# Performance work log

Hardware: AMD Instinct MI355X
Metric: run time of the kernel (lower is better)

The kernel has to match this reference:

```python
import jax, jax.numpy as jnp
import numpy as np

_SAMPLING_EPS = 1e-5


def setup_inputs() -> dict:
    key = jax.random.key(0)
    ks = jax.random.split(key, 7)
    N, V, H = 256, 128000, 200  # num_seqs, vocab_size, output-history length
    logits = jax.random.normal(ks[0], (N, V), dtype=jnp.float32)
    output_tokens = jax.random.randint(ks[1], (N, H), 0, V, dtype=jnp.int32)
    presence_penalties = jax.random.uniform(ks[2], (N,), jnp.float32, 0.0, 2.0)
    frequency_penalties = jax.random.uniform(ks[3], (N,), jnp.float32, 0.0, 2.0)
    temperatures = jax.random.uniform(ks[4], (N,), jnp.float32, 0.5, 1.5)
    top_ps = jax.random.uniform(ks[5], (N,), jnp.float32, 0.5, 1.0)
    top_ks = jax.random.randint(ks[6], (N,), 1, 1000, dtype=jnp.int32)
    return {
        "logits": logits,
        "presence_penalties": presence_penalties,
        "frequency_penalties": frequency_penalties,
        "temperatures": temperatures,
        "top_ps": top_ps,
        "output_tokens": output_tokens,
        "top_ks": top_ks,
    }


def reference(logits, presence_penalties, frequency_penalties, temperatures,
              top_ps, output_tokens, top_ks):
    N, V = logits.shape

    # ---- _apply_penalties: bincount of previously generated tokens per row ----
    rows = jnp.arange(N)[:, None]  # [N,1] broadcast against [N,H] token ids
    bin_counts = jnp.zeros((N, V), logits.dtype).at[rows, output_tokens].add(1.0)
    # rows are skipped when both penalties are < eps (original builds an index list)
    active = ((presence_penalties >= _SAMPLING_EPS) |
              (frequency_penalties >= _SAMPLING_EPS))[:, None]
    presence_mask = (bin_counts > 0.0).astype(logits.dtype)
    penalty = (frequency_penalties[:, None] * bin_counts
               + presence_penalties[:, None] * presence_mask)
    logits = logits - jnp.where(active, penalty, jnp.zeros((), logits.dtype))

    # ---- temperature scaling + softmax ----
    logits = logits / temperatures[:, None]
    probs = jax.nn.softmax(logits, axis=-1)

    # ---- _apply_top_p_top_k: sort desc, cumsum, mask, unsort ----
    probs_idx = jnp.argsort(-probs, axis=-1)                    # descending order
    probs_sort = jnp.take_along_axis(probs, probs_idx, axis=-1)
    probs_sum = jnp.cumsum(probs_sort, axis=-1)
    top_p_mask = (probs_sum - probs_sort) > top_ps[:, None]     # exclusive cumsum > p
    probs_sort = jnp.where(top_p_mask, 0.0, probs_sort)
    top_k_mask = jnp.arange(V, dtype=top_ks.dtype)[None, :] >= top_ks[:, None]
    probs_sort = jnp.where(top_k_mask, 0.0, probs_sort)
    inv_idx = jnp.argsort(probs_idx, axis=-1)                   # unsort permutation
    filtered_probs = jnp.take_along_axis(probs_sort, inv_idx, axis=-1)
    return filtered_probs
```

## Files before the change

kernel.cpp:

```cpp
#include <hip/hip_runtime.h>
#include <stdint.h>

#define NB 8192
#define BSHIFT 19
#define HS 512
#define HM 511
#define CAP 4096
#define CAP2 6144
#define PCAP 2048
#define NRB 2048
#define NT 1024
#define CAPTHR 1.75f

typedef unsigned long long ull;

__device__ __forceinline__ void bar_lds() {
    asm volatile("s_waitcnt lgkmcnt(0)" ::: "memory");
    __builtin_amdgcn_s_barrier();
    __builtin_amdgcn_sched_barrier(0);
}

__device__ __forceinline__ unsigned mono_u32(float x) {
    unsigned b = __float_as_uint(x);
    return (b & 0x80000000u) ? ~b : (b | 0x80000000u);
}
__device__ __forceinline__ float inv_mono(unsigned u) {
    unsigned b = (u & 0x80000000u) ? (u & 0x7fffffffu) : ~u;
    return __uint_as_float(b);
}

__device__ __forceinline__ float compute_x(float l, int cnt,
                                           float pres, float freq, float t) {
    float pen = __fadd_rn(__fmul_rn(freq, (float)cnt), (cnt > 0) ? pres : 0.0f);
    return __fdiv_rn(__fsub_rn(l, pen), t);
}

#define SHFL_STAGE(kk, jj) do {                                              \
    int _s = (jj) >> 1;                                                      \
    ull _pA = __shfl_xor(A, _s), _pB = __shfl_xor(B, _s);                    \
    bool _keepmn = (((e0 & (jj)) == 0) == ((e0 & (kk)) != 0));               \
    ull _mnA = (A < _pA) ? A : _pA, _mxA = (A < _pA) ? _pA : A;              \
    ull _mnB = (B < _pB) ? B : _pB, _mxB = (B < _pB) ? _pB : B;              \
    A = _keepmn ? _mnA : _mxA;  B = _keepmn ? _mnB : _mxB;                   \
} while (0)
#define PAIR_STAGE(kk) do {                                                  \
    bool _up = ((e0 & (kk)) != 0);                                           \
    ull _mn = (A < B) ? A : B, _mx = (A < B) ? B : A;                        \
    A = _up ? _mn : _mx;  B = _up ? _mx : _mn;                               \
} while (0)
#define ZDRIB(nn) do {                                                       \
    for (int _z = 0; _z < (nn) && zc < ZITER; ++_z) {                        \
        int _p = tid + zc * NT; if (_p < V4) o4p[_p] = z4; ++zc;             \
    }                                                                        \
} while (0)

__global__ __launch_bounds__(NT) void k_fused(
    const float* __restrict__ logits, const int* __restrict__ tokens,
    const float* __restrict__ pres_v, const float* __restrict__ freq_v,
    const float* __restrict__ temps, const float* __restrict__ topp_v,
    const int* __restrict__ topk_v, int V, int H, float* __restrict__ out)
{
    __shared__ __align__(16) char smem[(32 + 16 + 8 + 4) * 1024];
    unsigned* hc = (unsigned*)smem;
    ull* skey = (ull*)smem;
    char* regB = smem + 32 * 1024;
    float* se = (float*)regB;
    ull* tmpc = (ull*)regB;
    char* regC = smem + 48 * 1024;
    unsigned* rh = (unsigned*)regC;
    unsigned* cbuf = (unsigned*)regB;
    char* regD = smem + 56 * 1024;
    int* hkey = (int*)regD;
    int* hval = (int*)(regD + 2 * 1024);
    __shared__ int wt_i[16];
    __shared__ float wt_f[16];
    __shared__ float esum_s, corr_s;
    __shared__ int bstar_s, lcnt_s, rb_s, pcnt_s, cap_s;

    int row = blockIdx.x, tid = threadIdx.x;
    int lane = tid & 63, wid = tid >> 6;
    for (int b = tid; b < NB; b += NT) hc[b] = 0u;
    if (tid == 0) {
        esum_s = 0.f; corr_s = 0.f; bstar_s = -1;
        lcnt_s = 0; rb_s = 0; pcnt_s = 0; cap_s = 0;
    }

    for (int i = tid; i < HS; i += NT) { hkey[i] = -1; hval[i] = 0; }
    __syncthreads();
    const int* trow = tokens + (size_t)row * H;
    for (int i = tid; i < H; i += NT) {
        int v = trow[i];
        unsigned h = ((unsigned)v * 2654435761u) >> 23;
        while (true) {
            int prev = atomicCAS(&hkey[h], -1, v);
            if (prev == -1 || prev == v) { atomicAdd(&hval[h], 1); break; }
            h = (h + 1) & HM;
        }
    }
    __syncthreads();

    float t = temps[row];
    float topp = topp_v[row];
    float r = __fdiv_rn(1.0f, t);
    const float* lrow = logits + (size_t)row * V;
    const float4* l4p = (const float4*)lrow;
    float4* o4p = (float4*)(out + (size_t)row * V);
    const float4 z4 = make_float4(0.f, 0.f, 0.f, 0.f);
    int V4 = V >> 2;
    int ZITER = (V4 + NT - 1) / NT;
    int zc = 0;

    float es = 0.0f;
    int i = tid;
    for (; i + 7 * NT < V4; i += 8 * NT) {
        float4 arr[8];
#pragma unroll
        for (int q = 0; q < 8; ++q) arr[q] = l4p[i + q * NT];
#pragma unroll
        for (int q = 0; q < 8; ++q) {
            int vb = (i + q * NT) << 2;
#pragma unroll
            for (int j = 0; j < 4; ++j) {
                float l = (&arr[q].x)[j];
                float x = __fmul_rn(l, r);
                atomicAdd(&hc[mono_u32(x) >> BSHIFT], 1u);
                es += __expf(x);
                if (l >= CAPTHR) {
                    int pos = atomicAdd(&cap_s, 1);
                    if (pos < CAP2) cbuf[pos] = (unsigned)(vb + j);
                }
            }
        }
    }
    for (; i < V4; i += NT) {
        float4 A4 = l4p[i];
#pragma unroll
        for (int j = 0; j < 4; ++j) {
            float l = (&A4.x)[j];
            float x = __fmul_rn(l, r);
            atomicAdd(&hc[mono_u32(x) >> BSHIFT], 1u);
            es += __expf(x);
            if (l >= CAPTHR) {
                int pos = atomicAdd(&cap_s, 1);
                if (pos < CAP2) cbuf[pos] = (unsigned)((i << 2) + j);
            }
        }
    }
    for (int v = (V4 << 2) + tid; v < V; v += NT) {
        float l = lrow[v];
        float x = __fmul_rn(l, r);
        atomicAdd(&hc[mono_u32(x) >> BSHIFT], 1u);
        es += __expf(x);
        if (l >= CAPTHR) {
            int pos = atomicAdd(&cap_s, 1);
            if (pos < CAP2) cbuf[pos] = (unsigned)v;
        }
    }
    for (int off = 32; off; off >>= 1) es += __shfl_down(es, off);
    if ((tid & 63) == 0) atomicAdd(&esum_s, es);
    __syncthreads();

    float pres = pres_v[row], freq = freq_v[row];
    int active = (pres >= 1e-5f) || (freq >= 1e-5f);
    float corr = 0.0f;
    if (active) {
        for (int s = tid; s < HS; s += NT) {
            int v = hkey[s];
            if (v >= 0) {
                int c = hval[s];
                float l = lrow[v];
                float x0 = __fmul_rn(l, r);
                float xp = compute_x(l, c, pres, freq, t);
                unsigned b0 = mono_u32(x0) >> BSHIFT;
                unsigned bp = mono_u32(xp) >> BSHIFT;
                if (b0 != bp) { atomicSub(&hc[b0], 1u); atomicAdd(&hc[bp], 1u); }
                corr += __expf(xp) - __expf(x0);
            }
        }
    }
    for (int off = 32; off; off >>= 1) corr += __shfl_down(corr, off);
    if ((tid & 63) == 0) atomicAdd(&corr_s, corr);
    __syncthreads();

    const int BPT = NB / NT;
    int base = tid * BPT;
    int acc = 0;
#pragma unroll
    for (int q = BPT - 1; q >= 0; --q) { acc += (int)hc[base + q]; hc[base + q] = (unsigned)acc; }
    int k = topk_v[row];
    {
        int v = acc;
#pragma unroll
        for (int off = 1; off < 64; off <<= 1) {
            int o = __shfl_down(v, off);
            if (lane + off < 64) v += o;
        }
        if (lane == 0) wt_i[wid] = v;
        __syncthreads();
        int above = v - acc;
#pragma unroll
        for (int w = 0; w < 16; ++w) if (w > wid) above += wt_i[w];
        int best = -1;
#pragma unroll
        for (int q = BPT - 1; q >= 0; --q)
            if ((int)hc[base + q] + above >= k) { best = base + q; break; }
        if (best >= 0) atomicMax(&bstar_s, best);
    }
    __syncthreads();
    int bst = bstar_s - 2;
    if (bst < 0) bst = 0;
    float Sp = esum_s + corr_s;
    int ccount = cap_s;
    __syncthreads();

    int lb = (int)(mono_u32(__fmul_rn(CAPTHR, r)) >> BSHIFT);
    bool skip_c = (ccount <= CAP2) && (lb < bst);

    if (skip_c) {
        unsigned myidx[6];
#pragma unroll
        for (int q = 0; q < 6; ++q) {
            int j2 = tid + q * NT;
            myidx[q] = (j2 < ccount) ? cbuf[j2] : 0xffffffffu;
        }
        float myl[6];
#pragma unroll
        for (int q = 0; q < 6; ++q)
            if (myidx[q] != 0xffffffffu) myl[q] = lrow[myidx[q]];
#pragma unroll
        for (int q = 0; q < 6; ++q) {
            if (myidx[q] != 0xffffffffu) {
                float l = myl[q];
                unsigned ua = mono_u32(__fmul_rn(l, r));
                if ((int)(ua >> BSHIFT) >= bst) {
                    unsigned ue = mono_u32(__fdiv_rn(l, t));
                    int pos = atomicAdd(&lcnt_s, 1);
                    if (pos < CAP)
                        skey[pos] = ((ull)ue << 32) | (unsigned)~myidx[q];
                }
            }
        }
    } else {
        i = tid;
        for (; i + 7 * NT < V4; i += 8 * NT) {
            float4 arr[8];
#pragma unroll
            for (int q = 0; q < 8; ++q) arr[q] = l4p[i + q * NT];
#pragma unroll
            for (int q = 0; q < 8; ++q) {
                int vb = (i + q * NT) << 2;
#pragma unroll
                for (int j = 0; j < 4; ++j) {
                    float l = (&arr[q].x)[j];
                    unsigned ua = mono_u32(__fmul_rn(l, r));
                    if ((int)(ua >> BSHIFT) >= bst) {
                        unsigned ue = mono_u32(__fdiv_rn(l, t));
                        int pos = atomicAdd(&lcnt_s, 1);
                        if (pos < CAP)
                            skey[pos] = ((ull)ue << 32) | (unsigned)~(unsigned)(vb + j);
                    }
                }
            }
        }
        for (; i < V4; i += NT) {
            float4 A4 = l4p[i];
#pragma unroll
            for (int j = 0; j < 4; ++j) {
                float l = (&A4.x)[j];
                unsigned ua = mono_u32(__fmul_rn(l, r));
                if ((int)(ua >> BSHIFT) >= bst) {
                    unsigned ue = mono_u32(__fdiv_rn(l, t));
                    int pos = atomicAdd(&lcnt_s, 1);
                    if (pos < CAP)
                        skey[pos] = ((ull)ue << 32) | (unsigned)~(unsigned)((i << 2) + j);
                }
            }
        }
        for (int v = (V4 << 2) + tid; v < V; v += NT) {
            float l = lrow[v];
            unsigned ua = mono_u32(__fmul_rn(l, r));
            if ((int)(ua >> BSHIFT) >= bst) {
                unsigned ue = mono_u32(__fdiv_rn(l, t));
                int pos = atomicAdd(&lcnt_s, 1);
                if (pos < CAP)
                    skey[pos] = ((ull)ue << 32) | (unsigned)~(unsigned)v;
            }
        }
    }
    __syncthreads();
    int count = lcnt_s; if (count > CAP) count = CAP;

    if (active) {
        for (int j = tid; j < count; j += NT) {
            unsigned idx = ~(unsigned)(skey[j] & 0xffffffffull);
            unsigned h = (idx * 2654435761u) >> 23;
            int c = 0;
            while (true) {
                int kk = hkey[h];
                if (kk == (int)idx) { c = hval[h]; break; }
                if (kk == -1) break;
                h = (h + 1) & HM;
            }
            if (c > 0) {
                float xp = compute_x(lrow[idx], c, pres, freq, t);
                skey[j] = ((ull)mono_u32(xp) << 32) | (unsigned)~idx;
            }
        }
    }
    ZDRIB(2); bar_lds();

    for (int g = tid; g < NRB; g += NT) rh[g] = 0u;
    ZDRIB(2); bar_lds();
    int gmin = bst << 6;
    for (int j = tid; j < count; j += NT) {
        unsigned u = (unsigned)(skey[j] >> 32);
        int rel = (int)(u >> 13) - gmin;
        rel = rel < 0 ? 0 : (rel > NRB - 1 ? NRB - 1 : rel);
        atomicAdd(&rh[rel], 1u);
    }
    ZDRIB(2); bar_lds();
    {
        int b2i = tid * 2;
        int a2 = (int)rh[b2i + 1];
        rh[b2i + 1] = (unsigned)a2;
        a2 += (int)rh[b2i];
        rh[b2i] = (unsigned)a2;
        int v = a2;
#pragma unroll
        for (int off = 1; off < 64; off <<= 1) {
            int o = __shfl_down(v, off);
            if (lane + off < 64) v += o;
        }
        if (lane == 0) wt_i[wid] = v;
        ZDRIB(2); bar_lds();
        int above = v - a2;
#pragma unroll
        for (int w = 0; w < 16; ++w) if (w > wid) above += wt_i[w];
        int best = -1;
        if ((int)rh[b2i + 1] + above >= k) best = b2i + 1;
        else if ((int)rh[b2i] + above >= k) best = b2i;
        if (best >= 0) atomicMax(&rb_s, best);
    }
    ZDRIB(2); bar_lds();
    int rb = rb_s;
    for (int j = tid; j < count; j += NT) {
        unsigned u = (unsigned)(skey[j] >> 32);
        int rel = (int)(u >> 13) - gmin;
        rel = rel < 0 ? 0 : (rel > NRB - 1 ? NRB - 1 : rel);
        if (rel >= rb) {
            int pos = atomicAdd(&pcnt_s, 1);
            if (pos < PCAP) tmpc[pos] = skey[j];
        }
    }
    ZDRIB(2); bar_lds();
    int count2 = pcnt_s;
    if (count2 <= PCAP) {
        for (int j = tid; j < count2; j += NT) skey[j] = tmpc[j];
        count = count2;
    }
    ZDRIB(2); bar_lds();

    if (count <= PCAP) {
        const int M = 2048;
        for (int j = count + tid; j < M; j += NT) skey[j] = 0ull;
        ZDRIB(2); bar_lds();
        int e0 = (wid << 7) + (lane << 1);
        ull A = skey[e0], B = skey[e0 + 1];
        ZDRIB(2);
        for (int kk = 2; kk <= 128; kk <<= 1) {
            for (int jj = kk >> 1; jj >= 2; jj >>= 1) SHFL_STAGE(kk, jj);
            PAIR_STAGE(kk);
        }
        for (int kk = 256; kk <= 2048; kk <<= 1) {
            skey[e0] = A; skey[e0 + 1] = B;
            ZDRIB(2); bar_lds();
            for (int jj = kk >> 1; jj >= 128; jj >>= 1) {
                for (int i2 = tid; i2 < M; i2 += NT) {
                    int ixj = i2 ^ jj;
                    if (ixj > i2) {
                        ull X = skey[i2], Y = skey[ixj];
                        bool up = ((i2 & kk) != 0);
                        if ((X > Y) == up) { skey[i2] = Y; skey[ixj] = X; }
                    }
                }
                ZDRIB(2); bar_lds();
            }
            A = skey[e0]; B = skey[e0 + 1];
            for (int jj = 64; jj >= 2; jj >>= 1) SHFL_STAGE(kk, jj);
            PAIR_STAGE(kk);
        }
        skey[e0] = A; skey[e0 + 1] = B;
    } else {
        int m = 1; while (m < count) m <<= 1;
        for (int j = count + tid; j < m; j += NT) skey[j] = 0ull;
        __syncthreads();
        for (int kk = 2; kk <= m; kk <<= 1) {
            for (int jj = kk >> 1; jj > 0; jj >>= 1) {
                for (int i2 = tid; i2 < m; i2 += NT) {
                    int ixj = i2 ^ jj;
                    if (ixj > i2) {
                        ull X = skey[i2], Y = skey[ixj];
                        bool up = ((i2 & kk) != 0);
                        if ((X > Y) == up) { skey[i2] = Y; skey[ixj] = X; }
                    }
                }
                __syncthreads();
            }
        }
    }

    for (; zc < ZITER; ++zc) {
        int p = tid + zc * NT;
        if (p < V4) o4p[p] = z4;
    }
    for (int v2 = (V4 << 2) + tid; v2 < V; v2 += NT)
        out[(size_t)row * V + v2] = 0.0f;
    __syncthreads();

    for (int j = tid; j < CAP; j += NT)
        se[j] = (j < count) ? __expf(inv_mono((unsigned)(skey[j] >> 32))) : 0.0f;
    __syncthreads();
    int j0 = tid << 2;
    float e0f = se[j0], e1 = se[j0 + 1], e2 = se[j0 + 2], e3 = se[j0 + 3];
    float c0 = e0f, c1 = c0 + e1, c2 = c1 + e2, c3 = c2 + e3;
    float vf = c3;
#pragma unroll
    for (int off = 1; off < 64; off <<= 1) {
        float o = __shfl_up(vf, off);
        if (lane >= off) vf += o;
    }
    if (lane == 63) wt_f[wid] = vf;
    __syncthreads();
    float pre = vf - c3;
#pragma unroll
    for (int w = 0; w < 16; ++w) if (w < wid) pre += wt_f[w];

    float pS = topp * Sp;
    float inc[4] = {pre + c0, pre + c1, pre + c2, pre + c3};
    float ee[4] = {e0f, e1, e2, e3};
#pragma unroll
    for (int q = 0; q < 4; ++q) {
        int j = j0 + q;
        if (j < count) {
            float e = ee[q];
            float excl = __fsub_rn(inc[q], e);
            if ((j < k) && (excl <= pS)) {
                unsigned idx = ~(unsigned)(skey[j] & 0xffffffffull);
                out[(size_t)row * V + idx] = __fdiv_rn(e, Sp);
            }
        }
    }
}

extern "C" void kernel_launch(void* const* d_in, const int* in_sizes, int n_in,
                              void* d_out, int out_size, void* d_ws, size_t ws_size,
                              hipStream_t stream) {
    const float* logits = (const float*)d_in[0];
    const float* pres   = (const float*)d_in[1];
    const float* freq   = (const float*)d_in[2];
    const float* temps  = (const float*)d_in[3];
    const float* topps  = (const float*)d_in[4];
    const int*   tokens = (const int*)d_in[5];
    const int*   topks  = (const int*)d_in[6];
    int N = in_sizes[1];
    int V = in_sizes[0] / N;
    int H = in_sizes[5] / N;
    float* out = (float*)d_out;

    k_fused<<<N, NT, 0, stream>>>(logits, tokens, pres, freq, temps, topps,
                                  topks, V, H, out);
}
```

Before: 275.1 us.

## Histogram only high-logit candidates, with full-histogram fallback when top-k underfilled

```diff
diff --git a/kernel.cpp b/kernel.cpp
--- a/kernel.cpp
+++ b/kernel.cpp
@@ -123,9 +123,9 @@
             for (int j = 0; j < 4; ++j) {
                 float l = (&arr[q].x)[j];
                 float x = __fmul_rn(l, r);
-                atomicAdd(&hc[mono_u32(x) >> BSHIFT], 1u);
                 es += __expf(x);
                 if (l >= CAPTHR) {
+                    atomicAdd(&hc[mono_u32(x) >> BSHIFT], 1u);
                     int pos = atomicAdd(&cap_s, 1);
                     if (pos < CAP2) cbuf[pos] = (unsigned)(vb + j);
                 }
@@ -138,9 +138,9 @@
         for (int j = 0; j < 4; ++j) {
             float l = (&A4.x)[j];
             float x = __fmul_rn(l, r);
-            atomicAdd(&hc[mono_u32(x) >> BSHIFT], 1u);
             es += __expf(x);
             if (l >= CAPTHR) {
+                atomicAdd(&hc[mono_u32(x) >> BSHIFT], 1u);
                 int pos = atomicAdd(&cap_s, 1);
                 if (pos < CAP2) cbuf[pos] = (unsigned)((i << 2) + j);
             }
@@ -149,9 +149,9 @@
     for (int v = (V4 << 2) + tid; v < V; v += NT) {
         float l = lrow[v];
         float x = __fmul_rn(l, r);
-        atomicAdd(&hc[mono_u32(x) >> BSHIFT], 1u);
         es += __expf(x);
         if (l >= CAPTHR) {
+            atomicAdd(&hc[mono_u32(x) >> BSHIFT], 1u);
             int pos = atomicAdd(&cap_s, 1);
             if (pos < CAP2) cbuf[pos] = (unsigned)v;
         }
@@ -171,50 +171,110 @@
                 float l = lrow[v];
                 float x0 = __fmul_rn(l, r);
                 float xp = compute_x(l, c, pres, freq, t);
-                unsigned b0 = mono_u32(x0) >> BSHIFT;
-                unsigned bp = mono_u32(xp) >> BSHIFT;
-                if (b0 != bp) { atomicSub(&hc[b0], 1u); atomicAdd(&hc[bp], 1u); }
+                if (l >= CAPTHR) {
+                    unsigned b0 = mono_u32(x0) >> BSHIFT;
+                    unsigned bp = mono_u32(xp) >> BSHIFT;
+                    if (b0 != bp) { atomicSub(&hc[b0], 1u); atomicAdd(&hc[bp], 1u); }
+                }
                 corr += __expf(xp) - __expf(x0);
             }
         }
     }
     for (int off = 32; off; off >>= 1) corr += __shfl_down(corr, off);
     if ((tid & 63) == 0) atomicAdd(&corr_s, corr);
-    __syncthreads();
+    ZDRIB(2); bar_lds();
 
     const int BPT = NB / NT;
     int base = tid * BPT;
+    unsigned cnt[8];
+#pragma unroll
+    for (int q = 0; q < 8; ++q) cnt[q] = hc[base + q];
     int acc = 0;
 #pragma unroll
-    for (int q = BPT - 1; q >= 0; --q) { acc += (int)hc[base + q]; hc[base + q] = (unsigned)acc; }
+    for (int q = 0; q < 8; ++q) acc += (int)cnt[q];
     int k = topk_v[row];
-    {
-        int v = acc;
+    int vscan = acc;
+#pragma unroll
+    for (int off = 1; off < 64; off <<= 1) {
+        int o = __shfl_down(vscan, off);
+        if (lane + off < 64) vscan += o;
+    }
+    if (lane == 0) wt_i[wid] = vscan;
+    ZDRIB(2); bar_lds();
+    int tot = 0;
+#pragma unroll
+    for (int w = 0; w < 16; ++w) tot += wt_i[w];
+    int above = vscan - acc;
+#pragma unroll
+    for (int w = 0; w < 16; ++w) if (w > wid) above += wt_i[w];
+    int fb = (tot < k);
+    if (!fb) {
+        int sfx = 0, best = -1;
+#pragma unroll
+        for (int q = BPT - 1; q >= 0; --q) {
+            sfx += (int)cnt[q];
+            if (sfx + above >= k) { best = base + q; break; }
+        }
+        if (best >= 0) atomicMax(&bstar_s, best);
+    } else {
+        for (int v2 = tid; v2 < V; v2 += NT) {
+            float l = lrow[v2];
+            if (!(l >= CAPTHR)) {
+                float x = __fmul_rn(l, r);
+                atomicAdd(&hc[mono_u32(x) >> BSHIFT], 1u);
+            }
+        }
+        bar_lds();
+        if (active) {
+            for (int s = tid; s < HS; s += NT) {
+                int vv = hkey[s];
+                if (vv >= 0) {
+                    float l = lrow[vv];
+                    if (!(l >= CAPTHR)) {
+                        int c = hval[s];
+                        float x0 = __fmul_rn(l, r);
+                        float xp = compute_x(l, c, pres, freq, t);
+                        unsigned b0 = mono_u32(x0) >> BSHIFT;
+                        unsigned bp = mono_u32(xp) >> BSHIFT;
+                        if (b0 != bp) { atomicSub(&hc[b0], 1u); atomicAdd(&hc[bp], 1u); }
+                    }
+                }
+            }
+        }
+        bar_lds();
+#pragma unroll
+        for (int q = 0; q < 8; ++q) cnt[q] = hc[base + q];
+        acc = 0;
+#pragma unroll
+        for (int q = 0; q < 8; ++q) acc += (int)cnt[q];
+        vscan = acc;
 #pragma unroll
         for (int off = 1; off < 64; off <<= 1) {
-            int o = __shfl_down(v, off);
-            if (lane + off < 64) v += o;
-        }
-        if (lane == 0) wt_i[wid] = v;
-        __syncthreads();
-        int above = v - acc;
+            int o = __shfl_down(vscan, off);
+            if (lane + off < 64) vscan += o;
+        }
+        if (lane == 0) wt_i[wid] = vscan;
+        bar_lds();
+        above = vscan - acc;
 #pragma unroll
         for (int w = 0; w < 16; ++w) if (w > wid) above += wt_i[w];
-        int best = -1;
-#pragma unroll
-        for (int q = BPT - 1; q >= 0; --q)
-            if ((int)hc[base + q] + above >= k) { best = base + q; break; }
+        int sfx = 0, best = -1;
+#pragma unroll
+        for (int q = BPT - 1; q >= 0; --q) {
+            sfx += (int)cnt[q];
+            if (sfx + above >= k) { best = base + q; break; }
+        }
         if (best >= 0) atomicMax(&bstar_s, best);
     }
-    __syncthreads();
+    ZDRIB(2); bar_lds();
     int bst = bstar_s - 2;
     if (bst < 0) bst = 0;
     float Sp = esum_s + corr_s;
     int ccount = cap_s;
-    __syncthreads();
+    ZDRIB(2); bar_lds();
 
     int lb = (int)(mono_u32(__fmul_rn(CAPTHR, r)) >> BSHIFT);
-    bool skip_c = (ccount <= CAP2) && (lb < bst);
+    bool skip_c = (ccount <= CAP2) && (lb < bst) && !fb;
 
     if (skip_c) {
         unsigned myidx[6];
@@ -287,7 +347,7 @@
             }
         }
     }
-    __syncthreads();
+    ZDRIB(2); bar_lds();
     int count = lcnt_s; if (count > CAP) count = CAP;
 
     if (active) {
@@ -333,12 +393,12 @@
         }
         if (lane == 0) wt_i[wid] = v;
         ZDRIB(2); bar_lds();
-        int above = v - a2;
-#pragma unroll
-        for (int w = 0; w < 16; ++w) if (w > wid) above += wt_i[w];
+        int above2 = v - a2;
+#pragma unroll
+        for (int w = 0; w < 16; ++w) if (w > wid) above2 += wt_i[w];
         int best = -1;
-        if ((int)rh[b2i + 1] + above >= k) best = b2i + 1;
-        else if ((int)rh[b2i] + above >= k) best = b2i;
+        if ((int)rh[b2i + 1] + above2 >= k) best = b2i + 1;
+        else if ((int)rh[b2i] + above2 >= k) best = b2i;
         if (best >= 0) atomicMax(&rb_s, best);
     }
     ZDRIB(2); bar_lds();
```

Result: slower. 280.9 us (+2.1%).

## Histogram only high-logit candidates with penalized keys and interleave output zeroing

Applied to the files above, without the earlier changes.

```diff
diff --git a/kernel.cpp b/kernel.cpp
--- a/kernel.cpp
+++ b/kernel.cpp
@@ -1,14 +1,13 @@
 #include <hip/hip_runtime.h>
 #include <stdint.h>
 
-#define NB 8192
+#define NBR 1024
+#define BASEB 0x1700
 #define BSHIFT 19
 #define HS 512
 #define HM 511
 #define CAP 4096
 #define CAP2 6144
-#define PCAP 2048
-#define NRB 2048
 #define NT 1024
 #define CAPTHR 1.75f
 
@@ -19,6 +18,11 @@
     __builtin_amdgcn_s_barrier();
     __builtin_amdgcn_sched_barrier(0);
 }
+__device__ __forceinline__ void bar_full() {
+    asm volatile("s_waitcnt vmcnt(0) lgkmcnt(0)" ::: "memory");
+    __builtin_amdgcn_s_barrier();
+    __builtin_amdgcn_sched_barrier(0);
+}
 
 __device__ __forceinline__ unsigned mono_u32(float x) {
     unsigned b = __float_as_uint(x);
@@ -27,6 +31,10 @@
 __device__ __forceinline__ float inv_mono(unsigned u) {
     unsigned b = (u & 0x80000000u) ? (u & 0x7fffffffu) : ~u;
     return __uint_as_float(b);
+}
+__device__ __forceinline__ int relb(unsigned m) {
+    int rel = (int)(m >> BSHIFT) - BASEB;
+    return rel < 0 ? 0 : (rel > NBR - 1 ? NBR - 1 : rel);
 }
 
 __device__ __forceinline__ float compute_x(float l, int cnt,
@@ -60,30 +68,21 @@
     const float* __restrict__ temps, const float* __restrict__ topp_v,
     const int* __restrict__ topk_v, int V, int H, float* __restrict__ out)
 {
-    __shared__ __align__(16) char smem[(32 + 16 + 8 + 4) * 1024];
-    unsigned* hc = (unsigned*)smem;
-    ull* skey = (ull*)smem;
-    char* regB = smem + 32 * 1024;
-    float* se = (float*)regB;
-    ull* tmpc = (ull*)regB;
-    char* regC = smem + 48 * 1024;
-    unsigned* rh = (unsigned*)regC;
-    unsigned* cbuf = (unsigned*)regB;
-    char* regD = smem + 56 * 1024;
-    int* hkey = (int*)regD;
-    int* hval = (int*)(regD + 2 * 1024);
+    __shared__ __align__(16) char smem[56 * 1024];
+    ull* cbuf = (ull*)smem;
+    float* se = (float*)(smem + 32 * 1024);
+    unsigned* hc = (unsigned*)(smem + 48 * 1024);
+    int* hkey = (int*)(smem + 52 * 1024);
+    int* hval = (int*)(smem + 54 * 1024);
     __shared__ int wt_i[16];
     __shared__ float wt_f[16];
     __shared__ float esum_s, corr_s;
-    __shared__ int bstar_s, lcnt_s, rb_s, pcnt_s, cap_s;
+    __shared__ int bstar_s, lcnt_s, cap_s;
 
     int row = blockIdx.x, tid = threadIdx.x;
     int lane = tid & 63, wid = tid >> 6;
-    for (int b = tid; b < NB; b += NT) hc[b] = 0u;
-    if (tid == 0) {
-        esum_s = 0.f; corr_s = 0.f; bstar_s = -1;
-        lcnt_s = 0; rb_s = 0; pcnt_s = 0; cap_s = 0;
-    }
+    hc[tid] = 0u;
+    if (tid == 0) { esum_s = 0.f; corr_s = 0.f; bstar_s = -1; lcnt_s = 0; cap_s = 0; }
 
     for (int i = tid; i < HS; i += NT) { hkey[i] = -1; hval[i] = 0; }
     __syncthreads();
@@ -99,8 +98,10 @@
     }
     __syncthreads();
 
-    float t = temps[row];
-    float topp = topp_v[row];
+    float t = temps[row], topp = topp_v[row];
+    float pres = pres_v[row], freq = freq_v[row];
+    int k = topk_v[row];
+    int active = (pres >= 1e-5f) || (freq >= 1e-5f);
     float r = __fdiv_rn(1.0f, t);
     const float* lrow = logits + (size_t)row * V;
     const float4* l4p = (const float4*)lrow;
@@ -110,58 +111,6 @@
     int ZITER = (V4 + NT - 1) / NT;
     int zc = 0;
 
-    float es = 0.0f;
-    int i = tid;
-    for (; i + 7 * NT < V4; i += 8 * NT) {
-        float4 arr[8];
-#pragma unroll
-        for (int q = 0; q < 8; ++q) arr[q] = l4p[i + q * NT];
-#pragma unroll
-        for (int q = 0; q < 8; ++q) {
-            int vb = (i + q * NT) << 2;
-#pragma unroll
-            for (int j = 0; j < 4; ++j) {
-                float l = (&arr[q].x)[j];
-                float x = __fmul_rn(l, r);
-                atomicAdd(&hc[mono_u32(x) >> BSHIFT], 1u);
-                es += __expf(x);
-                if (l >= CAPTHR) {
-                    int pos = atomicAdd(&cap_s, 1);
-                    if (pos < CAP2) cbuf[pos] = (unsigned)(vb + j);
-                }
-            }
-        }
-    }
-    for (; i < V4; i += NT) {
-        float4 A4 = l4p[i];
-#pragma unroll
-        for (int j = 0; j < 4; ++j) {
-            float l = (&A4.x)[j];
-            float x = __fmul_rn(l, r);
-            atomicAdd(&hc[mono_u32(x) >> BSHIFT], 1u);
-            es += __expf(x);
-            if (l >= CAPTHR) {
-                int pos = atomicAdd(&cap_s, 1);
-                if (pos < CAP2) cbuf[pos] = (unsigned)((i << 2) + j);
-            }
-        }
-    }
-    for (int v = (V4 << 2) + tid; v < V; v += NT) {
-        float l = lrow[v];
-        float x = __fmul_rn(l, r);
-        atomicAdd(&hc[mono_u32(x) >> BSHIFT], 1u);
-        es += __expf(x);
-        if (l >= CAPTHR) {
-            int pos = atomicAdd(&cap_s, 1);
-            if (pos < CAP2) cbuf[pos] = (unsigned)v;
-        }
-    }
-    for (int off = 32; off; off >>= 1) es += __shfl_down(es, off);
-    if ((tid & 63) == 0) atomicAdd(&esum_s, es);
-    __syncthreads();
-
-    float pres = pres_v[row], freq = freq_v[row];
-    int active = (pres >= 1e-5f) || (freq >= 1e-5f);
     float corr = 0.0f;
     if (active) {
         for (int s = tid; s < HS; s += NT) {
@@ -169,12 +118,8 @@
             if (v >= 0) {
                 int c = hval[s];
                 float l = lrow[v];
-                float x0 = __fmul_rn(l, r);
-                float xp = compute_x(l, c, pres, freq, t);
-                unsigned b0 = mono_u32(x0) >> BSHIFT;
-                unsigned bp = mono_u32(xp) >> BSHIFT;
-                if (b0 != bp) { atomicSub(&hc[b0], 1u); atomicAdd(&hc[bp], 1u); }
-                corr += __expf(xp) - __expf(x0);
+                corr += __expf(compute_x(l, c, pres, freq, t))
+                      - __expf(__fmul_rn(l, r));
             }
         }
     }
@@ -182,244 +127,269 @@
     if ((tid & 63) == 0) atomicAdd(&corr_s, corr);
     __syncthreads();
 
-    const int BPT = NB / NT;
-    int base = tid * BPT;
-    int acc = 0;
-#pragma unroll
-    for (int q = BPT - 1; q >= 0; --q) { acc += (int)hc[base + q]; hc[base + q] = (unsigned)acc; }
-    int k = topk_v[row];
-    {
-        int v = acc;
-#pragma unroll
-        for (int off = 1; off < 64; off <<= 1) {
-            int o = __shfl_down(v, off);
-            if (lane + off < 64) v += o;
-        }
-        if (lane == 0) wt_i[wid] = v;
-        __syncthreads();
-        int above = v - acc;
-#pragma unroll
-        for (int w = 0; w < 16; ++w) if (w > wid) above += wt_i[w];
-        int best = -1;
-#pragma unroll
-        for (int q = BPT - 1; q >= 0; --q)
-            if ((int)hc[base + q] + above >= k) { best = base + q; break; }
-        if (best >= 0) atomicMax(&bstar_s, best);
-    }
-    __syncthreads();
-    int bst = bstar_s - 2;
-    if (bst < 0) bst = 0;
+    float es = 0.0f;
+    int i = tid;
+    for (; i + 7 * NT < V4; i += 8 * NT) {
+        float4 arr[8];
+#pragma unroll
+        for (int q = 0; q < 8; ++q) arr[q] = l4p[i + q * NT];
+        __builtin_amdgcn_sched_barrier(0);
+        ZDRIB(8);
+#pragma unroll
+        for (int q = 0; q < 8; ++q) {
+            int vb = (i + q * NT) << 2;
+#pragma unroll
+            for (int j = 0; j < 4; ++j) {
+                float l = (&arr[q].x)[j];
+                es += __expf(__fmul_rn(l, r));
+                if (l >= CAPTHR) {
+                    unsigned idx = (unsigned)(vb + j);
+                    int c = 0;
+                    if (active) {
+                        unsigned h = (idx * 2654435761u) >> 23;
+                        while (true) {
+                            int kk2 = hkey[h];
+                            if (kk2 == (int)idx) { c = hval[h]; break; }
+                            if (kk2 == -1) break;
+                            h = (h + 1) & HM;
+                        }
+                    }
+                    float xe = (c > 0) ? compute_x(l, c, pres, freq, t)
+                                       : __fdiv_rn(l, t);
+                    unsigned ue = mono_u32(xe);
+                    atomicAdd(&hc[relb(ue)], 1u);
+                    int pos = atomicAdd(&cap_s, 1);
+                    if (pos < CAP2) cbuf[pos] = ((ull)ue << 32) | (unsigned)~idx;
+                }
+            }
+        }
+    }
+    for (; i < V4; i += NT) {
+        float4 A4 = l4p[i];
+        __builtin_amdgcn_sched_barrier(0);
+        ZDRIB(2);
+#pragma unroll
+        for (int j = 0; j < 4; ++j) {
+            float l = (&A4.x)[j];
+            es += __expf(__fmul_rn(l, r));
+            if (l >= CAPTHR) {
+                unsigned idx = (unsigned)((i << 2) + j);
+                int c = 0;
+                if (active) {
+                    unsigned h = (idx * 2654435761u) >> 23;
+                    while (true) {
+                        int kk2 = hkey[h];
+                        if (kk2 == (int)idx) { c = hval[h]; break; }
+                        if (kk2 == -1) break;
+                        h = (h + 1) & HM;
+                    }
+                }
+                float xe = (c > 0) ? compute_x(l, c, pres, freq, t)
+                                   : __fdiv_rn(l, t);
+                unsigned ue = mono_u32(xe);
+                atomicAdd(&hc[relb(ue)], 1u);
+                int pos = atomicAdd(&cap_s, 1);
+                if (pos < CAP2) cbuf[pos] = ((ull)ue << 32) | (unsigned)~idx;
+            }
+        }
+    }
+    for (int v = (V4 << 2) + tid; v < V; v += NT) {
+        float l = lrow[v];
+        es += __expf(__fmul_rn(l, r));
+        if (l >= CAPTHR) {
+            unsigned idx = (unsigned)v;
+            int c = 0;
+            if (active) {
+                unsigned h = (idx * 2654435761u) >> 23;
+                while (true) {
+                    int kk2 = hkey[h];
+                    if (kk2 == (int)idx) { c = hval[h]; break; }
+                    if (kk2 == -1) break;
+                    h = (h + 1) & HM;
+                }
+            }
+            float xe = (c > 0) ? compute_x(l, c, pres, freq, t) : __fdiv_rn(l, t);
+            unsigned ue = mono_u32(xe);
+            atomicAdd(&hc[relb(ue)], 1u);
+            int pos = atomicAdd(&cap_s, 1);
+            if (pos < CAP2) cbuf[pos] = ((ull)ue << 32) | (unsigned)~idx;
+        }
+    }
+    for (; zc < ZITER; ++zc) { int p = tid + zc * NT; if (p < V4) o4p[p] = z4; }
+    for (int v2 = (V4 << 2) + tid; v2 < V; v2 += NT) out[(size_t)row * V + v2] = 0.0f;
+
+    for (int off = 32; off; off >>= 1) es += __shfl_down(es, off);
+    if ((tid & 63) == 0) atomicAdd(&esum_s, es);
+    bar_lds();
+
+    int myc = (int)hc[tid];
+    int vscan = myc;
+#pragma unroll
+    for (int off = 1; off < 64; off <<= 1) {
+        int o = __shfl_down(vscan, off);
+        if (lane + off < 64) vscan += o;
+    }
+    if (lane == 0) wt_i[wid] = vscan;
+    bar_lds();
+    int tot = 0;
+#pragma unroll
+    for (int w = 0; w < 16; ++w) tot += wt_i[w];
+    int above = vscan - myc;
+#pragma unroll
+    for (int w = 0; w < 16; ++w) if (w > wid) above += wt_i[w];
+    int fb = (tot < k);
+    if (!fb && (myc + above >= k)) atomicMax(&bstar_s, tid);
+    bar_lds();
+    int bst_rel = bstar_s; if (bst_rel < 0) bst_rel = 0;
     float Sp = esum_s + corr_s;
     int ccount = cap_s;
-    __syncthreads();
-
-    int lb = (int)(mono_u32(__fmul_rn(CAPTHR, r)) >> BSHIFT);
-    bool skip_c = (ccount <= CAP2) && (lb < bst);
+    int lb_rel = relb(mono_u32(__fdiv_rn(CAPTHR, t)));
+    bool skip_c = (!fb) && (ccount <= CAP2) && (lb_rel < bst_rel);
+    unsigned bst_abs = (unsigned)(bst_rel + BASEB);
+    int count;
 
     if (skip_c) {
-        unsigned myidx[6];
+        int base6 = tid * 6;
+        ull pr[6]; int sb[6]; int svc = 0;
 #pragma unroll
         for (int q = 0; q < 6; ++q) {
-            int j2 = tid + q * NT;
-            myidx[q] = (j2 < ccount) ? cbuf[j2] : 0xffffffffu;
-        }
-        float myl[6];
-#pragma unroll
-        for (int q = 0; q < 6; ++q)
-            if (myidx[q] != 0xffffffffu) myl[q] = lrow[myidx[q]];
-#pragma unroll
-        for (int q = 0; q < 6; ++q) {
-            if (myidx[q] != 0xffffffffu) {
-                float l = myl[q];
-                unsigned ua = mono_u32(__fmul_rn(l, r));
-                if ((int)(ua >> BSHIFT) >= bst) {
-                    unsigned ue = mono_u32(__fdiv_rn(l, t));
-                    int pos = atomicAdd(&lcnt_s, 1);
-                    if (pos < CAP)
-                        skey[pos] = ((ull)ue << 32) | (unsigned)~myidx[q];
-                }
-            }
-        }
+            int j2 = base6 + q;
+            bool in = (j2 < ccount);
+            pr[q] = in ? cbuf[j2] : 0ull;
+            int s = (in && (((unsigned)(pr[q] >> 32)) >> BSHIFT) >= bst_abs) ? 1 : 0;
+            sb[q] = s; svc += s;
+        }
+        bar_lds();
+        int vs = svc;
+#pragma unroll
+        for (int off = 1; off < 64; off <<= 1) {
+            int o = __shfl_up(vs, off);
+            if (lane >= off) vs += o;
+        }
+        if (lane == 63) wt_i[wid] = vs;
+        bar_lds();
+        int pre = vs - svc;
+#pragma unroll
+        for (int w = 0; w < 16; ++w) if (w < wid) pre += wt_i[w];
+        int total = 0;
+#pragma unroll
+        for (int w = 0; w < 16; ++w) total += wt_i[w];
+        int pos = pre;
+#pragma unroll
+        for (int q = 0; q < 6; ++q) if (sb[q]) cbuf[pos++] = pr[q];
+        count = total > CAP ? CAP : total;
+        bar_lds();
     } else {
-        i = tid;
-        for (; i + 7 * NT < V4; i += 8 * NT) {
-            float4 arr[8];
-#pragma unroll
-            for (int q = 0; q < 8; ++q) arr[q] = l4p[i + q * NT];
-#pragma unroll
-            for (int q = 0; q < 8; ++q) {
-                int vb = (i + q * NT) << 2;
-#pragma unroll
-                for (int j = 0; j < 4; ++j) {
-                    float l = (&arr[q].x)[j];
-                    unsigned ua = mono_u32(__fmul_rn(l, r));
-                    if ((int)(ua >> BSHIFT) >= bst) {
-                        unsigned ue = mono_u32(__fdiv_rn(l, t));
-                        int pos = atomicAdd(&lcnt_s, 1);
-                        if (pos < CAP)
-                            skey[pos] = ((ull)ue << 32) | (unsigned)~(unsigned)(vb + j);
+        if (fb) {
+            for (int v = tid; v < V; v += NT) {
+                float l = lrow[v];
+                if (!(l >= CAPTHR)) {
+                    int c = 0;
+                    if (active) {
+                        unsigned h = ((unsigned)v * 2654435761u) >> 23;
+                        while (true) {
+                            int kk2 = hkey[h];
+                            if (kk2 == v) { c = hval[h]; break; }
+                            if (kk2 == -1) break;
+                            h = (h + 1) & HM;
+                        }
                     }
-                }
-            }
-        }
-        for (; i < V4; i += NT) {
-            float4 A4 = l4p[i];
-#pragma unroll
-            for (int j = 0; j < 4; ++j) {
-                float l = (&A4.x)[j];
-                unsigned ua = mono_u32(__fmul_rn(l, r));
-                if ((int)(ua >> BSHIFT) >= bst) {
-                    unsigned ue = mono_u32(__fdiv_rn(l, t));
-                    int pos = atomicAdd(&lcnt_s, 1);
-                    if (pos < CAP)
-                        skey[pos] = ((ull)ue << 32) | (unsigned)~(unsigned)((i << 2) + j);
-                }
-            }
-        }
-        for (int v = (V4 << 2) + tid; v < V; v += NT) {
+                    float xe = (c > 0) ? compute_x(l, c, pres, freq, t) : __fdiv_rn(l, t);
+                    atomicAdd(&hc[relb(mono_u32(xe))], 1u);
+                }
+            }
+            bar_lds();
+            myc = (int)hc[tid];
+            vscan = myc;
+#pragma unroll
+            for (int off = 1; off < 64; off <<= 1) {
+                int o = __shfl_down(vscan, off);
+                if (lane + off < 64) vscan += o;
+            }
+            if (lane == 0) wt_i[wid] = vscan;
+            bar_lds();
+            above = vscan - myc;
+#pragma unroll
+            for (int w = 0; w < 16; ++w) if (w > wid) above += wt_i[w];
+            if (myc + above >= k) atomicMax(&bstar_s, tid);
+            bar_lds();
+            bst_rel = bstar_s < 0 ? 0 : bstar_s;
+        }
+        for (int v = tid; v < V; v += NT) {
             float l = lrow[v];
-            unsigned ua = mono_u32(__fmul_rn(l, r));
-            if ((int)(ua >> BSHIFT) >= bst) {
-                unsigned ue = mono_u32(__fdiv_rn(l, t));
+            int c = 0;
+            if (active) {
+                unsigned h = ((unsigned)v * 2654435761u) >> 23;
+                while (true) {
+                    int kk2 = hkey[h];
+                    if (kk2 == v) { c = hval[h]; break; }
+                    if (kk2 == -1) break;
+                    h = (h + 1) & HM;
+                }
+            }
+            float xe = (c > 0) ? compute_x(l, c, pres, freq, t) : __fdiv_rn(l, t);
+            unsigned ue = mono_u32(xe);
+            if (relb(ue) >= bst_rel) {
                 int pos = atomicAdd(&lcnt_s, 1);
-                if (pos < CAP)
-                    skey[pos] = ((ull)ue << 32) | (unsigned)~(unsigned)v;
-            }
-        }
-    }
-    __syncthreads();
-    int count = lcnt_s; if (count > CAP) count = CAP;
-
-    if (active) {
-        for (int j = tid; j < count; j += NT) {
-            unsigned idx = ~(unsigned)(skey[j] & 0xffffffffull);
-            unsigned h = (idx * 2654435761u) >> 23;
-            int c = 0;
-            while (true) {
-                int kk = hkey[h];
-                if (kk == (int)idx) { c = hval[h]; break; }
-                if (kk == -1) break;
-                h = (h + 1) & HM;
-            }
-            if (c > 0) {
-                float xp = compute_x(lrow[idx], c, pres, freq, t);
-                skey[j] = ((ull)mono_u32(xp) << 32) | (unsigned)~idx;
-            }
-        }
-    }
-    ZDRIB(2); bar_lds();
-
-    for (int g = tid; g < NRB; g += NT) rh[g] = 0u;
-    ZDRIB(2); bar_lds();
-    int gmin = bst << 6;
-    for (int j = tid; j < count; j += NT) {
-        unsigned u = (unsigned)(skey[j] >> 32);
-        int rel = (int)(u >> 13) - gmin;
-        rel = rel < 0 ? 0 : (rel > NRB - 1 ? NRB - 1 : rel);
-        atomicAdd(&rh[rel], 1u);
-    }
-    ZDRIB(2); bar_lds();
-    {
-        int b2i = tid * 2;
-        int a2 = (int)rh[b2i + 1];
-        rh[b2i + 1] = (unsigned)a2;
-        a2 += (int)rh[b2i];
-        rh[b2i] = (unsigned)a2;
-        int v = a2;
-#pragma unroll
-        for (int off = 1; off < 64; off <<= 1) {
-            int o = __shfl_down(v, off);
-            if (lane + off < 64) v += o;
-        }
-        if (lane == 0) wt_i[wid] = v;
-        ZDRIB(2); bar_lds();
-        int above = v - a2;
-#pragma unroll
-        for (int w = 0; w < 16; ++w) if (w > wid) above += wt_i[w];
-        int best = -1;
-        if ((int)rh[b2i + 1] + above >= k) best = b2i + 1;
-        else if ((int)rh[b2i] + above >= k) best = b2i;
-        if (best >= 0) atomicMax(&rb_s, best);
-    }
-    ZDRIB(2); bar_lds();
-    int rb = rb_s;
-    for (int j = tid; j < count; j += NT) {
-        unsigned u = (unsigned)(skey[j] >> 32);
-        int rel = (int)(u >> 13) - gmin;
-        rel = rel < 0 ? 0 : (rel > NRB - 1 ? NRB - 1 : rel);
-        if (rel >= rb) {
-            int pos = atomicAdd(&pcnt_s, 1);
-            if (pos < PCAP) tmpc[pos] = skey[j];
-        }
-    }
-    ZDRIB(2); bar_lds();
-    int count2 = pcnt_s;
-    if (count2 <= PCAP) {
-        for (int j = tid; j < count2; j += NT) skey[j] = tmpc[j];
-        count = count2;
-    }
-    ZDRIB(2); bar_lds();
-
-    if (count <= PCAP) {
+                if (pos < CAP) cbuf[pos] = ((ull)ue << 32) | (unsigned)~(unsigned)v;
+            }
+        }
+        bar_lds();
+        count = lcnt_s > CAP ? CAP : lcnt_s;
+    }
+
+    if (count <= 2048) {
         const int M = 2048;
-        for (int j = count + tid; j < M; j += NT) skey[j] = 0ull;
-        ZDRIB(2); bar_lds();
+        for (int j = count + tid; j < M; j += NT) cbuf[j] = 0ull;
+        bar_lds();
         int e0 = (wid << 7) + (lane << 1);
-        ull A = skey[e0], B = skey[e0 + 1];
-        ZDRIB(2);
+        ull A = cbuf[e0], B = cbuf[e0 + 1];
         for (int kk = 2; kk <= 128; kk <<= 1) {
             for (int jj = kk >> 1; jj >= 2; jj >>= 1) SHFL_STAGE(kk, jj);
             PAIR_STAGE(kk);
         }
         for (int kk = 256; kk <= 2048; kk <<= 1) {
-            skey[e0] = A; skey[e0 + 1] = B;
-            ZDRIB(2); bar_lds();
+            cbuf[e0] = A; cbuf[e0 + 1] = B;
+            bar_lds();
             for (int jj = kk >> 1; jj >= 128; jj >>= 1) {
                 for (int i2 = tid; i2 < M; i2 += NT) {
                     int ixj = i2 ^ jj;
                     if (ixj > i2) {
-                        ull X = skey[i2], Y = skey[ixj];
+                        ull X = cbuf[i2], Y = cbuf[ixj];
                         bool up = ((i2 & kk) != 0);
-                        if ((X > Y) == up) { skey[i2] = Y; skey[ixj] = X; }
+                        if ((X > Y) == up) { cbuf[i2] = Y; cbuf[ixj] = X; }
                     }
                 }
-                ZDRIB(2); bar_lds();
-            }
-            A = skey[e0]; B = skey[e0 + 1];
+                bar_lds();
+            }
+            A = cbuf[e0]; B = cbuf[e0 + 1];
             for (int jj = 64; jj >= 2; jj >>= 1) SHFL_STAGE(kk, jj);
             PAIR_STAGE(kk);
         }
-        skey[e0] = A; skey[e0 + 1] = B;
+        cbuf[e0] = A; cbuf[e0 + 1] = B;
+        bar_lds();
     } else {
         int m = 1; while (m < count) m <<= 1;
-        for (int j = count + tid; j < m; j += NT) skey[j] = 0ull;
-        __syncthreads();
+        for (int j = count + tid; j < m; j += NT) cbuf[j] = 0ull;
+        bar_lds();
         for (int kk = 2; kk <= m; kk <<= 1) {
             for (int jj = kk >> 1; jj > 0; jj >>= 1) {
                 for (int i2 = tid; i2 < m; i2 += NT) {
                     int ixj = i2 ^ jj;
                     if (ixj > i2) {
-                        ull X = skey[i2], Y = skey[ixj];
+                        ull X = cbuf[i2], Y = cbuf[ixj];
                         bool up = ((i2 & kk) != 0);
-                        if ((X > Y) == up) { skey[i2] = Y; skey[ixj] = X; }
+                        if ((X > Y) == up) { cbuf[i2] = Y; cbuf[ixj] = X; }
                     }
                 }
-                __syncthreads();
-            }
-        }
-    }
-
-    for (; zc < ZITER; ++zc) {
-        int p = tid + zc * NT;
-        if (p < V4) o4p[p] = z4;
-    }
-    for (int v2 = (V4 << 2) + tid; v2 < V; v2 += NT)
-        out[(size_t)row * V + v2] = 0.0f;
-    __syncthreads();
+                bar_lds();
+            }
+        }
+    }
 
     for (int j = tid; j < CAP; j += NT)
-        se[j] = (j < count) ? __expf(inv_mono((unsigned)(skey[j] >> 32))) : 0.0f;
-    __syncthreads();
+        se[j] = (j < count) ? __expf(inv_mono((unsigned)(cbuf[j] >> 32))) : 0.0f;
+    bar_lds();
     int j0 = tid << 2;
     float e0f = se[j0], e1 = se[j0 + 1], e2 = se[j0 + 2], e3 = se[j0 + 3];
     float c0 = e0f, c1 = c0 + e1, c2 = c1 + e2, c3 = c2 + e3;
@@ -430,10 +400,12 @@
         if (lane >= off) vf += o;
     }
     if (lane == 63) wt_f[wid] = vf;
-    __syncthreads();
+    bar_lds();
     float pre = vf - c3;
 #pragma unroll
     for (int w = 0; w < 16; ++w) if (w < wid) pre += wt_f[w];
+
+    bar_full();
 
     float pS = topp * Sp;
     float inc[4] = {pre + c0, pre + c1, pre + c2, pre + c3};
@@ -445,7 +417,7 @@
             float e = ee[q];
             float excl = __fsub_rn(inc[q], e);
             if ((j < k) && (excl <= pS)) {
-                unsigned idx = ~(unsigned)(skey[j] & 0xffffffffull);
+                unsigned idx = ~(unsigned)(cbuf[j] & 0xffffffffull);
                 out[(size_t)row * V + idx] = __fdiv_rn(e, Sp);
             }
         }
```

After: 305.0 us. +10.9%, slower.
